# Performance work log

Measured on AMD Instinct MI355X. Metric: run time of the kernel, lower is better.

## Reference

```python
import jax, jax.numpy as jnp
import numpy as np

H = 32          # hidden_dim
N_LAYERS = 3
W_SCALE = 0.15  # keep tanh out of saturation (mimics uniform(-1/sqrt(H)) init scale)


def setup_inputs() -> dict:
    key = jax.random.key(0)
    ks = jax.random.split(key, 8)
    B, T, D = 512, 2048, 6
    return {
        "x": jax.random.normal(ks[0], (B, T, D), dtype=jnp.float32),
        "W_ih0": jax.random.normal(ks[1], (H, D), dtype=jnp.float32) * W_SCALE,
        "W_ih_rest": jax.random.normal(ks[2], (N_LAYERS - 1, H, H), dtype=jnp.float32) * W_SCALE,
        "W_hh": jax.random.normal(ks[3], (N_LAYERS, H, H), dtype=jnp.float32) * W_SCALE,
        "b_ih": jax.random.normal(ks[4], (N_LAYERS, H), dtype=jnp.float32) * W_SCALE,
        "b_hh": jax.random.normal(ks[5], (N_LAYERS, H), dtype=jnp.float32) * W_SCALE,
        "fc_w": jax.random.normal(ks[6], (6, H), dtype=jnp.float32) * W_SCALE,
        "fc_b": jax.random.normal(ks[7], (6,), dtype=jnp.float32) * W_SCALE,
    }


def _rnn_layer(seq, W_ih, W_hh_l, b_ih_l, b_hh_l):
    # seq: [B, T, in]; precompute the input projection for all timesteps (one big GEMM),
    # then scan only carries the tiny h @ W_hh recurrence.
    B = seq.shape[0]
    pre = jnp.einsum('bti,hi->bth', seq, W_ih) + b_ih_l + b_hh_l  # [B, T, H]
    pre_t = jnp.swapaxes(pre, 0, 1)  # [T, B, H] for scan over time

    def step(h, p_t):
        h_new = jnp.tanh(p_t + h @ W_hh_l.T)
        return h_new, h_new

    h0 = jnp.zeros((B, H), dtype=seq.dtype)
    h_last, hs = jax.lax.scan(step, h0, pre_t)
    return jnp.swapaxes(hs, 0, 1), h_last  # [B, T, H], [B, H]


def reference(x, W_ih0, W_ih_rest, W_hh, b_ih, b_hh, fc_w, fc_b):
    seq = x
    h_last = None
    for l in range(N_LAYERS):
        W_ih = W_ih0 if l == 0 else W_ih_rest[l - 1]
        seq, h_last = _rnn_layer(seq, W_ih, W_hh[l], b_ih[l], b_hh[l])
    # h_n[-1] -> final hidden state of last layer, then linear head
    return h_last @ fc_w.T + fc_b  # [B, n_classes]
```

## Files before the change

kernel.cpp:

```cpp
#include <hip/hip_runtime.h>


#define T_LEN 2048
#define D_IN  6
#define KS    8
#define NPH   (T_LEN / KS)

typedef float f4 __attribute__((ext_vector_type(4)));
typedef unsigned int u2 __attribute__((ext_vector_type(2)));

#if defined(__has_builtin)
#  if __has_builtin(__builtin_amdgcn_permlane32_swap)
#    define HAVE_PLSWAP 1
#  endif
#endif

__device__ __forceinline__ float xhalf_sum(float c) {
#ifdef HAVE_PLSWAP
    u2 r = __builtin_amdgcn_permlane32_swap(__float_as_uint(c), __float_as_uint(c),
                                            false, false);
    return __uint_as_float(r.x) + __uint_as_float(r.y);
#else
    return c + __shfl_xor(c, 32, 64);
#endif
}

__device__ __forceinline__ float fast_tanh(float v) {
    float e = __expf(2.0f * v);
    float r = __builtin_amdgcn_rcpf(e + 1.0f);
    return __builtin_fmaf(-2.0f, r, 1.0f);
}

__device__ __forceinline__ float rl(float v, int srclane) {
    return __int_as_float(__builtin_amdgcn_readlane(__float_as_int(v), srclane));
}

__global__ void __launch_bounds__(192) rnn3_lds(
    const float* __restrict__ x,
    const float* __restrict__ Wih0,
    const float* __restrict__ WihR,
    const float* __restrict__ Whh,
    const float* __restrict__ bih,
    const float* __restrict__ bhh,
    const float* __restrict__ fcw,
    const float* __restrict__ fcb,
    float* __restrict__ out)
{
    const int b    = blockIdx.x;
    const int tid  = threadIdx.x;
    const int wid  = tid >> 6;
    const int lane = tid & 63;
    const int j    = lane & 31;
    const int p    = lane >> 5;

    __shared__ __align__(16) float ring[3][2][KS][64];

    float wh[16];
    {
        const f4* q4 = (const f4*)(Whh + wid * 1024 + j * 32 + 16 * p);
        f4 q0 = q4[0], q1 = q4[1], q2 = q4[2], q3 = q4[3];
#pragma unroll
        for (int i = 0; i < 4; ++i) {
            wh[i] = q0[i]; wh[4 + i] = q1[i]; wh[8 + i] = q2[i]; wh[12 + i] = q3[i];
        }
    }
    const float bs = bih[wid * 32 + j] + bhh[wid * 32 + j];

    float wi[16];
    float w0x[D_IN];
    if (wid == 0) {
#pragma unroll
        for (int d = 0; d < D_IN; ++d) w0x[d] = Wih0[j * D_IN + d];
    } else {
        const f4* q4 = (const f4*)(WihR + (wid - 1) * 1024 + j * 32 + 16 * p);
        f4 q0 = q4[0], q1 = q4[1], q2 = q4[2], q3 = q4[3];
#pragma unroll
        for (int i = 0; i < 4; ++i) {
            wi[i] = q0[i]; wi[4 + i] = q1[i]; wi[8 + i] = q2[i]; wi[12 + i] = q3[i];
        }
    }

    ring[wid][1][KS - 1][lane] = 0.0f;

    const float* xg = x + (size_t)b * (T_LEN * D_IN);
    float xcur = 0.0f, xnext = 0.0f;
    if (wid == 0 && lane < KS * D_IN) xcur = xg[lane];

#pragma unroll 1
    for (int ph = 0; ph < NPH + 2; ++ph) {
        const int q = ph - wid;
        if (q >= 0 && q < NPH) {
            const int qb = q & 1;
            float (*selfb)[64] = ring[wid][qb];
            float (*selfp)[64] = ring[wid][qb ^ 1];

            if (wid == 0) {
                float xa[KS];
#pragma unroll
                for (int s = 0; s < KS; ++s) {
                    float acc = bs;
#pragma unroll
                    for (int d = 0; d < D_IN; ++d)
                        acc += rl(xcur, s * D_IN + d) * w0x[d];
                    xa[s] = acc;
                }
                if (q + 1 < NPH && lane < KS * D_IN)
                    xnext = xg[(q + 1) * (KS * D_IN) + lane];

#pragma unroll
                for (int s = 0; s < KS; ++s) {
                    const float* hp = (s == 0) ? &selfp[KS - 1][16 * p]
                                               : &selfb[s - 1][16 * p];
                    const f4* h4 = (const f4*)hp;
                    f4 h0 = h4[0], h1 = h4[1], h2 = h4[2], h3v = h4[3];
                    float a0 = 0.f, a1 = 0.f, a2 = 0.f, a3 = 0.f;
#pragma unroll
                    for (int i = 0; i < 4; ++i) {
                        a0 += h0[i] * wh[i];
                        a1 += h1[i] * wh[4 + i];
                        a2 += h2[i] * wh[8 + i];
                        a3 += h3v[i] * wh[12 + i];
                    }
                    float part = (a0 + a1) + (a2 + a3);
                    float h = fast_tanh(xhalf_sum(part) + xa[s]);
                    selfb[s][lane] = h;
                }
                xcur = xnext;
            } else {
                float (*srcb)[64] = ring[wid - 1][qb];
#pragma unroll
                for (int s = 0; s < KS; ++s) {
                    const f4* c4 = (const f4*)&srcb[s][16 * p];
                    f4 c0 = c4[0], c1 = c4[1], c2 = c4[2], c3 = c4[3];
                    const float* hp = (s == 0) ? &selfp[KS - 1][16 * p]
                                               : &selfb[s - 1][16 * p];
                    const f4* h4 = (const f4*)hp;
                    f4 h0 = h4[0], h1 = h4[1], h2 = h4[2], h3v = h4[3];
                    float a0 = 0.f, a1 = 0.f, a2 = 0.f, a3 = 0.f;
#pragma unroll
                    for (int i = 0; i < 4; ++i) {
                        a0 += c0[i] * wi[i];
                        a1 += c1[i] * wi[4 + i];
                        a2 += c2[i] * wi[8 + i];
                        a3 += c3[i] * wi[12 + i];
                    }
#pragma unroll
                    for (int i = 0; i < 4; ++i) {
                        a0 += h0[i] * wh[i];
                        a1 += h1[i] * wh[4 + i];
                        a2 += h2[i] * wh[8 + i];
                        a3 += h3v[i] * wh[12 + i];
                    }
                    float part = (a0 + a1) + (a2 + a3);
                    float h = fast_tanh(xhalf_sum(part) + bs);
                    selfb[s][lane] = h;
                }
            }
        }
        __syncthreads();
    }

    if (wid == 2 && lane < D_IN) {
        const float* h3 = ring[2][(NPH - 1) & 1][KS - 1];
        float acc = fcb[lane];
        const f4* fw = (const f4*)(fcw + lane * 32);
        const f4* hv = (const f4*)h3;
#pragma unroll
        for (int m = 0; m < 8; ++m) {
            f4 w4 = fw[m], hh = hv[m];
#pragma unroll
            for (int i = 0; i < 4; ++i) acc += hh[i] * w4[i];
        }
        out[b * D_IN + lane] = acc;
    }
}

extern "C" void kernel_launch(void* const* d_in, const int* in_sizes, int n_in,
                              void* d_out, int out_size, void* d_ws, size_t ws_size,
                              hipStream_t stream) {
    const float* x    = (const float*)d_in[0];
    const float* Wih0 = (const float*)d_in[1];
    const float* WihR = (const float*)d_in[2];
    const float* Whh  = (const float*)d_in[3];
    const float* bih  = (const float*)d_in[4];
    const float* bhh  = (const float*)d_in[5];
    const float* fcw  = (const float*)d_in[6];
    const float* fcb  = (const float*)d_in[7];
    float* outp = (float*)d_out;

    const int B = in_sizes[0] / (T_LEN * D_IN);
    rnn3_lds<<<B, 192, 0, stream>>>(x, Wih0, WihR, Whh, bih, bhh, fcw, fcb, outp);
}
```

Baseline: 474.4 us.

## Keep recurrent hidden state in registers and exchange it with DPP row rotations

The per-step recurrent matvec now reads the previous hidden state from registers through DPP row_ror rotations and permlane swaps, instead of reading it back from LDS. Weights are pre-permuted per lane to match the rotation order. LDS is used only for the handoff between layers, and the layer-0 input projection is staged and computed one phase ahead. The aim is to take LDS load latency off the serial dependency chain, at the cost of more cross-lane ops per step and a reliance on runtime detection of the rotation direction.

```diff
diff --git a/kernel.cpp b/kernel.cpp
--- a/kernel.cpp
+++ b/kernel.cpp
@@ -7,23 +7,16 @@
 #define NPH   (T_LEN / KS)
 
 typedef float f4 __attribute__((ext_vector_type(4)));
-typedef unsigned int u2 __attribute__((ext_vector_type(2)));
+typedef unsigned int u2v __attribute__((ext_vector_type(2)));
 
 #if defined(__has_builtin)
+#  if __has_builtin(__builtin_amdgcn_permlane16_swap)
+#    define HAVE_PL16 1
+#  endif
 #  if __has_builtin(__builtin_amdgcn_permlane32_swap)
-#    define HAVE_PLSWAP 1
+#    define HAVE_PL32 1
 #  endif
 #endif
-
-__device__ __forceinline__ float xhalf_sum(float c) {
-#ifdef HAVE_PLSWAP
-    u2 r = __builtin_amdgcn_permlane32_swap(__float_as_uint(c), __float_as_uint(c),
-                                            false, false);
-    return __uint_as_float(r.x) + __uint_as_float(r.y);
-#else
-    return c + __shfl_xor(c, 32, 64);
-#endif
-}
 
 __device__ __forceinline__ float fast_tanh(float v) {
     float e = __expf(2.0f * v);
@@ -31,11 +24,51 @@
     return __builtin_fmaf(-2.0f, r, 1.0f);
 }
 
-__device__ __forceinline__ float rl(float v, int srclane) {
-    return __int_as_float(__builtin_amdgcn_readlane(__float_as_int(v), srclane));
-}
-
-__global__ void __launch_bounds__(192) rnn3_lds(
+__device__ __forceinline__ float xhalf16(float c) {
+#ifdef HAVE_PL16
+    u2v r = __builtin_amdgcn_permlane16_swap(__float_as_uint(c), __float_as_uint(c),
+                                             false, false);
+    return __uint_as_float(r.x) + __uint_as_float(r.y);
+#else
+    return c + __shfl_xor(c, 16, 64);
+#endif
+}
+
+__device__ __forceinline__ float other32(float v) {
+#ifdef HAVE_PL32
+    u2v r = __builtin_amdgcn_permlane32_swap(__float_as_uint(v), __float_as_uint(v),
+                                             false, false);
+    return __uint_as_float(r.x ^ r.y ^ __float_as_uint(v));
+#else
+    return __shfl_xor(v, 32, 64);
+#endif
+}
+
+template<int R>
+__device__ __forceinline__ float rot16(float v) {
+    if constexpr (R == 0) return v;
+    else return __int_as_float(__builtin_amdgcn_update_dpp(
+        0, __float_as_int(v), 0x120 | R, 0xF, 0xF, true));
+}
+template<int R>
+__device__ __forceinline__ int rot16i(int v) {
+    if constexpr (R == 0) return v;
+    else return __builtin_amdgcn_update_dpp(0, v, 0x120 | R, 0xF, 0xF, true);
+}
+
+#define SELF4(r0, r1, r2, r3)                                   \
+    a0 = __builtin_fmaf(rot16<r0>(hs), ws[r0], a0);             \
+    a1 = __builtin_fmaf(rot16<r1>(hs), ws[r1], a1);             \
+    a2 = __builtin_fmaf(rot16<r2>(hs), ws[r2], a2);             \
+    a3 = __builtin_fmaf(rot16<r3>(hs), ws[r3], a3);
+
+#define CROSS4(r0, r1, r2, r3)                                  \
+    a0 = __builtin_fmaf(rot16<r0>(hxv), wx[r0], a0);            \
+    a1 = __builtin_fmaf(rot16<r1>(hxv), wx[r1], a1);            \
+    a2 = __builtin_fmaf(rot16<r2>(hxv), wx[r2], a2);            \
+    a3 = __builtin_fmaf(rot16<r3>(hxv), wx[r3], a3);
+
+__global__ void __launch_bounds__(192) rnn3_dpp2(
     const float* __restrict__ x,
     const float* __restrict__ Wih0,
     const float* __restrict__ WihR,
@@ -46,132 +79,156 @@
     const float* __restrict__ fcb,
     float* __restrict__ out)
 {
-    const int b    = blockIdx.x;
-    const int tid  = threadIdx.x;
-    const int wid  = tid >> 6;
-    const int lane = tid & 63;
-    const int j    = lane & 31;
-    const int p    = lane >> 5;
-
-    __shared__ __align__(16) float ring[3][2][KS][64];
-
-    float wh[16];
+    const int b   = blockIdx.x;
+    const int tid = threadIdx.x;
+    const int wid = tid >> 6;
+    const int L   = tid & 63;
+    const int low = L & 15;
+    const int b4  = (L >> 4) & 1;
+    const int b5  = L >> 5;
+    const int j   = 16 * b5 + low;
+    const int j0  = L & 31;
+
+    __shared__ float ring[2][2][KS][32];
+    __shared__ float h3buf[32];
+    __shared__ __align__(16) float xstage[KS * D_IN];
+    __shared__ float xap[2][KS][32];
+
+    const int probe = __builtin_amdgcn_readfirstlane(rot16i<1>(low));
+    const int dir   = (probe == 15) ? -1 : 1;
+
+    float ws[16];
     {
-        const f4* q4 = (const f4*)(Whh + wid * 1024 + j * 32 + 16 * p);
-        f4 q0 = q4[0], q1 = q4[1], q2 = q4[2], q3 = q4[3];
+        const float* row = Whh + wid * 1024 + j * 32;
+#pragma unroll
+        for (int r = 0; r < 16; ++r) ws[r] = row[16 * b4 + ((low + dir * r) & 15)];
+    }
+    float wx[16];
+    if (wid > 0) {
+        const float* row = WihR + (wid - 1) * 1024 + j * 32;
+#pragma unroll
+        for (int r = 0; r < 16; ++r) wx[r] = row[16 * b4 + ((low + dir * r) & 15)];
+    }
+    const float bsj = bih[wid * 32 + j] + bhh[wid * 32 + j];
+
+    const int sblk = b5;
+    float w0c[D_IN];
+    float bs0 = 0.0f;
+    if (wid == 0) {
+#pragma unroll
+        for (int d = 0; d < D_IN; ++d) w0c[d] = Wih0[j0 * D_IN + d];
+        bs0 = bih[j0] + bhh[j0];
+    }
+
+    const float* xg = x + (size_t)b * (T_LEN * D_IN);
+    float xld = 0.0f;
+
+    if (wid == 0) {
+        if (L < KS * D_IN) xstage[L] = xg[L];
+        float Xf[24];
+        {
+            const f4* xs = (const f4*)&xstage[24 * sblk];
+            f4 v0 = xs[0], v1 = xs[1], v2 = xs[2], v3 = xs[3], v4 = xs[4], v5 = xs[5];
+#pragma unroll
+            for (int i = 0; i < 4; ++i) {
+                Xf[i] = v0[i]; Xf[4 + i] = v1[i]; Xf[8 + i] = v2[i];
+                Xf[12 + i] = v3[i]; Xf[16 + i] = v4[i]; Xf[20 + i] = v5[i];
+            }
+        }
 #pragma unroll
         for (int i = 0; i < 4; ++i) {
-            wh[i] = q0[i]; wh[4 + i] = q1[i]; wh[8 + i] = q2[i]; wh[12 + i] = q3[i];
-        }
-    }
-    const float bs = bih[wid * 32 + j] + bhh[wid * 32 + j];
-
-    float wi[16];
-    float w0x[D_IN];
-    if (wid == 0) {
-#pragma unroll
-        for (int d = 0; d < D_IN; ++d) w0x[d] = Wih0[j * D_IN + d];
-    } else {
-        const f4* q4 = (const f4*)(WihR + (wid - 1) * 1024 + j * 32 + 16 * p);
-        f4 q0 = q4[0], q1 = q4[1], q2 = q4[2], q3 = q4[3];
-#pragma unroll
-        for (int i = 0; i < 4; ++i) {
-            wi[i] = q0[i]; wi[4 + i] = q1[i]; wi[8 + i] = q2[i]; wi[12 + i] = q3[i];
-        }
-    }
-
-    ring[wid][1][KS - 1][lane] = 0.0f;
-
-    const float* xg = x + (size_t)b * (T_LEN * D_IN);
-    float xcur = 0.0f, xnext = 0.0f;
-    if (wid == 0 && lane < KS * D_IN) xcur = xg[lane];
+            float acc = bs0;
+#pragma unroll
+            for (int d = 0; d < D_IN; ++d)
+                acc = __builtin_fmaf(Xf[6 * i + d], w0c[d], acc);
+            xap[0][4 * sblk + i][j0] = acc;
+        }
+        if (NPH > 1 && L < KS * D_IN) xld = xg[KS * D_IN + L];
+    }
+
+    float hs = 0.0f;
+    const bool needswap = (b4 != b5);
 
 #pragma unroll 1
     for (int ph = 0; ph < NPH + 2; ++ph) {
         const int q = ph - wid;
         if (q >= 0 && q < NPH) {
             const int qb = q & 1;
-            float (*selfb)[64] = ring[wid][qb];
-            float (*selfp)[64] = ring[wid][qb ^ 1];
-
             if (wid == 0) {
-                float xa[KS];
+                float xabuf[KS];
+#pragma unroll
+                for (int s = 0; s < KS; ++s) xabuf[s] = xap[qb][s][j];
 #pragma unroll
                 for (int s = 0; s < KS; ++s) {
-                    float acc = bs;
-#pragma unroll
-                    for (int d = 0; d < D_IN; ++d)
-                        acc += rl(xcur, s * D_IN + d) * w0x[d];
-                    xa[s] = acc;
+                    float a0 = 0.f, a1 = 0.f, a2 = 0.f, a3 = 0.f;
+                    SELF4(0, 1, 2, 3) SELF4(4, 5, 6, 7)
+                    SELF4(8, 9, 10, 11) SELF4(12, 13, 14, 15)
+                    float full = xhalf16((a0 + a1) + (a2 + a3));
+                    float h = fast_tanh(full + xabuf[s]);
+                    if (!b4) ring[0][qb][s][j] = h;
+                    float o = other32(h);
+                    hs = needswap ? o : h;
                 }
-                if (q + 1 < NPH && lane < KS * D_IN)
-                    xnext = xg[(q + 1) * (KS * D_IN) + lane];
-
+                if (q + 1 < NPH) {
+                    if (L < KS * D_IN) xstage[L] = xld;
+                    float Xf[24];
+                    {
+                        const f4* xs = (const f4*)&xstage[24 * sblk];
+                        f4 v0 = xs[0], v1 = xs[1], v2 = xs[2], v3 = xs[3], v4 = xs[4], v5 = xs[5];
+#pragma unroll
+                        for (int i = 0; i < 4; ++i) {
+                            Xf[i] = v0[i]; Xf[4 + i] = v1[i]; Xf[8 + i] = v2[i];
+                            Xf[12 + i] = v3[i]; Xf[16 + i] = v4[i]; Xf[20 + i] = v5[i];
+                        }
+                    }
+#pragma unroll
+                    for (int i = 0; i < 4; ++i) {
+                        float acc = bs0;
+#pragma unroll
+                        for (int d = 0; d < D_IN; ++d)
+                            acc = __builtin_fmaf(Xf[6 * i + d], w0c[d], acc);
+                        xap[qb ^ 1][4 * sblk + i][j0] = acc;
+                    }
+                    if (q + 2 < NPH && L < KS * D_IN)
+                        xld = xg[(q + 2) * (KS * D_IN) + L];
+                }
+            } else {
+                float hxbuf[KS];
+#pragma unroll
+                for (int s = 0; s < KS; ++s) hxbuf[s] = ring[wid - 1][qb][s][j0];
 #pragma unroll
                 for (int s = 0; s < KS; ++s) {
-                    const float* hp = (s == 0) ? &selfp[KS - 1][16 * p]
-                                               : &selfb[s - 1][16 * p];
-                    const f4* h4 = (const f4*)hp;
-                    f4 h0 = h4[0], h1 = h4[1], h2 = h4[2], h3v = h4[3];
+                    const float hxv = hxbuf[s];
                     float a0 = 0.f, a1 = 0.f, a2 = 0.f, a3 = 0.f;
-#pragma unroll
-                    for (int i = 0; i < 4; ++i) {
-                        a0 += h0[i] * wh[i];
-                        a1 += h1[i] * wh[4 + i];
-                        a2 += h2[i] * wh[8 + i];
-                        a3 += h3v[i] * wh[12 + i];
-                    }
-                    float part = (a0 + a1) + (a2 + a3);
-                    float h = fast_tanh(xhalf_sum(part) + xa[s]);
-                    selfb[s][lane] = h;
-                }
-                xcur = xnext;
-            } else {
-                float (*srcb)[64] = ring[wid - 1][qb];
-#pragma unroll
-                for (int s = 0; s < KS; ++s) {
-                    const f4* c4 = (const f4*)&srcb[s][16 * p];
-                    f4 c0 = c4[0], c1 = c4[1], c2 = c4[2], c3 = c4[3];
-                    const float* hp = (s == 0) ? &selfp[KS - 1][16 * p]
-                                               : &selfb[s - 1][16 * p];
-                    const f4* h4 = (const f4*)hp;
-                    f4 h0 = h4[0], h1 = h4[1], h2 = h4[2], h3v = h4[3];
-                    float a0 = 0.f, a1 = 0.f, a2 = 0.f, a3 = 0.f;
-#pragma unroll
-                    for (int i = 0; i < 4; ++i) {
-                        a0 += c0[i] * wi[i];
-                        a1 += c1[i] * wi[4 + i];
-                        a2 += c2[i] * wi[8 + i];
-                        a3 += c3[i] * wi[12 + i];
-                    }
-#pragma unroll
-                    for (int i = 0; i < 4; ++i) {
-                        a0 += h0[i] * wh[i];
-                        a1 += h1[i] * wh[4 + i];
-                        a2 += h2[i] * wh[8 + i];
-                        a3 += h3v[i] * wh[12 + i];
-                    }
-                    float part = (a0 + a1) + (a2 + a3);
-                    float h = fast_tanh(xhalf_sum(part) + bs);
-                    selfb[s][lane] = h;
+                    SELF4(0, 1, 2, 3)   CROSS4(0, 1, 2, 3)
+                    SELF4(4, 5, 6, 7)   CROSS4(4, 5, 6, 7)
+                    SELF4(8, 9, 10, 11) CROSS4(8, 9, 10, 11)
+                    SELF4(12, 13, 14, 15) CROSS4(12, 13, 14, 15)
+                    float full = xhalf16((a0 + a1) + (a2 + a3));
+                    float h = fast_tanh(full + bsj);
+                    if (wid == 1 && !b4) ring[1][qb][s][j] = h;
+                    float o = other32(h);
+                    hs = needswap ? o : h;
                 }
             }
         }
         __syncthreads();
     }
 
-    if (wid == 2 && lane < D_IN) {
-        const float* h3 = ring[2][(NPH - 1) & 1][KS - 1];
-        float acc = fcb[lane];
-        const f4* fw = (const f4*)(fcw + lane * 32);
-        const f4* hv = (const f4*)h3;
-#pragma unroll
-        for (int m = 0; m < 8; ++m) {
-            f4 w4 = fw[m], hh = hv[m];
-#pragma unroll
-            for (int i = 0; i < 4; ++i) acc += hh[i] * w4[i];
-        }
-        out[b * D_IN + lane] = acc;
+    if (wid == 2) {
+        if (L < 32) h3buf[L] = hs;
+        if (L < D_IN) {
+            float acc = fcb[L];
+            const f4* fw = (const f4*)(fcw + L * 32);
+            const f4* hv = (const f4*)h3buf;
+#pragma unroll
+            for (int m = 0; m < 8; ++m) {
+                f4 w4 = fw[m], h4 = hv[m];
+#pragma unroll
+                for (int i = 0; i < 4; ++i) acc = __builtin_fmaf(h4[i], w4[i], acc);
+            }
+            out[b * D_IN + L] = acc;
+        }
     }
 }
 
@@ -189,5 +246,5 @@
     float* outp = (float*)d_out;
 
     const int B = in_sizes[0] / (T_LEN * D_IN);
-    rnn3_lds<<<B, 192, 0, stream>>>(x, Wih0, WihR, Whh, bih, bhh, fcw, fcb, outp);
-}
+    rnn3_dpp2<<<B, 192, 0, stream>>>(x, Wih0, WihR, Whh, bih, bhh, fcw, fcb, outp);
+}
```

Measured after the change: 645.6 us. 1.36x slower.
